# Optimization experiments

Measured on AMD Instinct MI355X. Metric: run time of the kernel, lower is better.

Reference implementation:

```python
import jax, jax.numpy as jnp
import numpy as np

B = 4096       # batch
N_IN = 784     # input neurons
BANKS = 64     # banks per layer
L = 16         # layers of banks (layer 0 = input banks)
FAN = 8        # fan-out per source bank into next layer
D = 10         # n_neurons_per_hidd_bank
N_CONN = (L - 1) * BANKS * FAN  # total bank connections (7680)


def setup_inputs() -> dict:
    key = jax.random.key(0)
    ks = jax.random.split(key, 7)
    x = jax.random.normal(ks[0], (B, N_IN), jnp.float32)
    # input2hidden: Linear(N_IN, D, bias=True) for each input bank -> weight [D, N_IN]
    Wi = jax.random.normal(ks[1], (BANKS, D, N_IN), jnp.float32) / np.sqrt(N_IN).astype(np.float32)
    bi = jax.random.normal(ks[2], (BANKS, D), jnp.float32) * 0.1
    # per-edge gate: Linear(D, 1, bias=True); bias shifted so gates are a mix of open/closed
    Wg = jax.random.normal(ks[3], (L - 1, BANKS, FAN, D), jnp.float32) / np.sqrt(D).astype(np.float32)
    bg = jax.random.normal(ks[4], (L - 1, BANKS, FAN), jnp.float32) * 0.3 + 0.2
    # per-edge data: Linear(D, D, bias=False) -> weight [out=D, in=D]
    Wd = jax.random.normal(ks[5], (L - 1, BANKS, FAN, D, D), jnp.float32) / np.sqrt(D).astype(np.float32)
    # hidden2output: Linear(D, 1, bias=False) per output bank
    Wo = jax.random.normal(ks[6], (BANKS, D), jnp.float32) / np.sqrt(D).astype(np.float32)
    return {"x": x, "Wi": Wi, "bi": bi, "Wg": Wg, "bg": bg, "Wd": Wd, "Wo": Wo}


def reference(x, Wi, bi, Wg, bg, Wd, Wo):
    # forward_softgate with defaults: no batch norm, dropout p=0 (identity),
    # gates enabled (b_no_gates=False), positive gate loss, no gate_status.
    batch = x.shape[0]
    # static scatter targets: source bank s feeds banks (s+k)%BANKS of next layer
    s = np.arange(BANKS)[:, None]
    k = np.arange(FAN)[None, :]
    tgt = jnp.asarray(((s + k) % BANKS).reshape(-1))  # [BANKS*FAN]

    # input banks (layer 0); the target loop applies ReLU to every bank, incl. input banks
    acts = jax.nn.relu(jnp.einsum('bi,koi->bko', x, Wi) + bi)  # [B, BANKS, D]

    def layer(acts, w):
        wg, bgl, wd = w
        # gate: hardtanh(Linear(acts), 0, 1) per edge -> [B, BANKS, FAN]
        gate = jnp.clip(jnp.einsum('bsd,skd->bsk', acts, wg) + bgl, 0.0, 1.0)
        # data: Linear(D, D, bias=False); torch y = x @ W.T with W[out, in]
        data = jnp.einsum('bsd,sked->bske', acts, wd)  # [B, BANKS, FAN, D]
        contrib = (gate[..., None] * data).reshape(batch, BANKS * FAN, D)
        acc = jnp.zeros_like(acts).at[:, tgt].add(contrib)  # scatter-add into target banks
        new_acts = jax.nn.relu(acc)
        gate_sum = gate.sum(axis=(1, 2))                   # per-sample gate activity
        n_open = (gate > 0.0).sum().astype(jnp.float32)    # open-gate count
        return new_acts, (gate_sum, n_open)

    acts, (gate_sums, n_opens) = jax.lax.scan(layer, acts, (Wg, bg, Wd))
    total_gate_act = (gate_sums.sum(axis=0) / N_CONN)[:, None]          # [B, 1]
    prob_open_gate = n_opens.sum() / (N_CONN * batch)                   # scalar
    # output banks = last layer banks, Linear(D,1,bias=False) each, then ReLU
    output = jax.nn.relu(jnp.einsum('bkd,kd->bk', acts, Wo))            # [B, BANKS]
    return output, total_gate_act, prob_open_gate
```

## Files before the change

kernel.cpp:

```cpp
#include <hip/hip_runtime.h>
#include <type_traits>

#define NIN 784
#define BANKS 64
#define NLAYER 15
#define FAN 8
#define DD 10
#define NBF 640
#define NSW 4
#define NSB 8

typedef float f32x2 __attribute__((ext_vector_type(2)));

#define BM 128
#define BN 64
#define BK 16

__global__ __launch_bounds__(256)
void input_gemm(const float* __restrict__ x, const float* __restrict__ Wi,
                const float* __restrict__ bi, float* __restrict__ acts)
{
    __shared__ float As[BK][BM + 4];
    __shared__ float Bs[BK][BN + 4];
    const int tid = threadIdx.x;
    const int tx = tid & 15, ty = tid >> 4;
    const int m0 = blockIdx.x * BM;
    const int n0 = blockIdx.y * BN;

    f32x2 acc2[8][2];
#pragma unroll
    for (int i = 0; i < 8; ++i)
#pragma unroll
        for (int j = 0; j < 2; ++j) acc2[i][j] = f32x2{0.f, 0.f};

    for (int kb = 0; kb < NIN / BK; ++kb) {
#pragma unroll
        for (int i = 0; i < 2; ++i) {
            int flat = tid + 256 * i;
            int m = flat >> 2, kq = flat & 3;
            float4 v = *(const float4*)(x + (m0 + m) * NIN + kb * BK + kq * 4);
            As[kq*4+0][m] = v.x; As[kq*4+1][m] = v.y;
            As[kq*4+2][m] = v.z; As[kq*4+3][m] = v.w;
        }
        {
            int n = tid >> 2, kq = tid & 3;
            float4 v = *(const float4*)(Wi + (n0 + n) * NIN + kb * BK + kq * 4);
            Bs[kq*4+0][n] = v.x; Bs[kq*4+1][n] = v.y;
            Bs[kq*4+2][n] = v.z; Bs[kq*4+3][n] = v.w;
        }
        __syncthreads();
#pragma unroll
        for (int k = 0; k < BK; ++k) {
            float4 a0 = *(const float4*)(&As[k][ty*8]);
            float4 a1 = *(const float4*)(&As[k][ty*8+4]);
            float4 bb = *(const float4*)(&Bs[k][tx*4]);
            float av[8] = {a0.x,a0.y,a0.z,a0.w,a1.x,a1.y,a1.z,a1.w};
            f32x2 bv2[2] = { f32x2{bb.x, bb.y}, f32x2{bb.z, bb.w} };
#pragma unroll
            for (int i = 0; i < 8; ++i) {
                f32x2 ai = f32x2{av[i], av[i]};
#pragma unroll
                for (int j = 0; j < 2; ++j)
                    acc2[i][j] = __builtin_elementwise_fma(ai, bv2[j], acc2[i][j]);
            }
        }
        __syncthreads();
    }
    float4 bv = *(const float4*)(bi + n0 + tx*4);
#pragma unroll
    for (int i = 0; i < 8; ++i) {
        int row = m0 + ty*8 + i;
        float4 o;
        o.x = fmaxf(acc2[i][0][0] + bv.x, 0.f);
        o.y = fmaxf(acc2[i][0][1] + bv.y, 0.f);
        o.z = fmaxf(acc2[i][1][0] + bv.z, 0.f);
        o.w = fmaxf(acc2[i][1][1] + bv.w, 0.f);
        *(float4*)(acts + row * NBF + n0 + tx*4) = o;
    }
}

__device__ __forceinline__ float f4c_rt(const float4& v, int c) {
    return c == 0 ? v.x : (c == 1 ? v.y : (c == 2 ? v.z : v.w));
}

typedef const __attribute__((address_space(1))) void gas_void;
typedef __attribute__((address_space(3))) void las_void;

__device__ __forceinline__ void gll16(const void* g, void* l) {
    __builtin_amdgcn_global_load_lds((gas_void*)g, (las_void*)l, 16, 0, 0);
}

#define NCH (NLAYER*FAN*28*64)
#define NBI (NLAYER*2*64)

__global__ __launch_bounds__(256)
void transpose_weights(const float* __restrict__ Wg, const float* __restrict__ bg,
                       const float* __restrict__ Wd,
                       float4* __restrict__ chunk_t, float4* __restrict__ bias_t)
{
    int tid = blockIdx.x * 256 + threadIdx.x;
    if (tid < NCH) {
        int b = tid & 63;
        int rk = tid >> 6;
        int r = rk % 28;
        int lk = rk / 28;
        int k = lk & 7;
        int l = lk >> 3;
        float4 v;
        if (r < 25) {
            v = ((const float4*)Wd)[(((size_t)(l*64+b)*8 + k)*25) + r];
        } else {
            int q = r - 25;
            size_t base = ((size_t)(l*64+b)*8 + k)*10 + 4*q;
            float t[4];
#pragma unroll
            for (int c = 0; c < 4; ++c)
                t[c] = (4*q + c < 10) ? Wg[base + c] : 0.f;
            v = make_float4(t[0], t[1], t[2], t[3]);
        }
        chunk_t[tid] = v;
    } else if (tid < NCH + NBI) {
        int t2 = tid - NCH;
        int b = t2 & 63;
        int q = (t2 >> 6) & 1;
        int l = t2 >> 7;
        bias_t[t2] = ((const float4*)bg)[(size_t)(l*64+b)*2 + q];
    }
}

__global__ __launch_bounds__(256, 2)
void routenet_v9(const float* __restrict__ acts0,
                 const float4* __restrict__ chunk_t, const float4* __restrict__ bias_t,
                 const float* __restrict__ Wo,
                 float* __restrict__ out, unsigned int* __restrict__ nopen_g)
{
    __shared__ float4 wdstage[2][28][64];
    __shared__ float4 biasbuf[2][2][64];
    __shared__ float  exch[2][NSW][5][64];

    const int tid  = threadIdx.x;
    const int lane = tid & 63;
    const int w    = tid >> 6;
    const int g    = w & 1;
    const int h    = w >> 1;
    const int b0   = blockIdx.x * NSB + g * NSW;

    f32x2 A2[2][DD];
#pragma unroll
    for (int p = 0; p < 2; ++p) {
        const float2* q0 = (const float2*)(acts0 + (size_t)(b0 + 2*p    ) * NBF + lane * DD);
        const float2* q1 = (const float2*)(acts0 + (size_t)(b0 + 2*p + 1) * NBF + lane * DD);
#pragma unroll
        for (int d2 = 0; d2 < 5; ++d2) {
            float2 v0 = q0[d2], v1 = q1[d2];
            A2[p][2*d2  ] = f32x2{v0.x, v1.x};
            A2[p][2*d2+1] = f32x2{v0.y, v1.y};
        }
    }

    f32x2 gs2[2] = { f32x2{0.f,0.f}, f32x2{0.f,0.f} };
    unsigned int nop = 0;

    auto stage_chunk = [&](int l, int k, int pdst) {
        const float4* base = chunk_t + (size_t)(l*8 + k) * 28 * 64;
#pragma unroll
        for (int j = 0; j < 7; ++j) {
            int r = w + 4 * j;
            gll16(base + r*64 + lane, &wdstage[pdst][r][0]);
        }
    };
    auto stage_bias = [&](int l) {
        int q = w & 1;
        gll16(bias_t + (size_t)(l*2 + q)*64 + lane, &biasbuf[l & 1][q][0]);
    };

    stage_chunk(0, 0, 0);
    stage_bias(0);
    asm volatile("s_waitcnt vmcnt(0)" ::: "memory");
    asm volatile("s_barrier" ::: "memory");

    for (int l = 0; l < NLAYER; ++l) {
        const int lp = l & 1;
        f32x2 acc2[2][5];
#pragma unroll
        for (int p = 0; p < 2; ++p)
#pragma unroll
            for (int el = 0; el < 5; ++el) acc2[p][el] = f32x2{0.f, 0.f};

        auto chunk_body = [&](auto Hc, int k, int p) {
            constexpr int H = Hc.value;
            float4 wgq[3];
#pragma unroll
            for (int q = 0; q < 3; ++q) wgq[q] = wdstage[p][25 + q][lane];
            const float bias = f4c_rt(biasbuf[lp][(k >> 2) & 1][lane], k & 3);
            float wgv[DD];
#pragma unroll
            for (int d = 0; d < DD; ++d) wgv[d] = f4c_rt(wgq[d >> 2], d & 3);

            f32x2 gz[2];
#pragma unroll
            for (int pp = 0; pp < 2; ++pp) {
                f32x2 z = f32x2{bias, bias};
#pragma unroll
                for (int d = 0; d < DD; ++d)
                    z = __builtin_elementwise_fma(A2[pp][d], f32x2{wgv[d], wgv[d]}, z);
                f32x2 gate = __builtin_elementwise_min(
                                 __builtin_elementwise_max(z, f32x2{0.f, 0.f}),
                                 f32x2{1.f, 1.f});
                if (H == 0) {
                    gs2[pp] += gate;
                    nop += (z[0] > 0.f) ? 1u : 0u;
                    nop += (z[1] > 0.f) ? 1u : 0u;
                }
                gz[pp] = gate;
            }

            float4 wv[13];
#pragma unroll
            for (int i = 0; i < 13; ++i) wv[i] = wdstage[p][12*H + i][lane];

            const int src = (lane - k) & 63;
#pragma unroll
            for (int el = 0; el < 5; ++el) {
#pragma unroll
                for (int pp = 0; pp < 2; ++pp) {
                    f32x2 dot = f32x2{0.f, 0.f};
#pragma unroll
                    for (int d = 0; d < DD; ++d) {
                        const int idx = (5*H + el) * 10 + d - 48*H;
                        const float wd = f4c_rt(wv[idx >> 2], idx & 3);
                        dot = __builtin_elementwise_fma(A2[pp][d], f32x2{wd, wd}, dot);
                    }
                    f32x2 cc = gz[pp] * dot;
                    f32x2 r;
                    r[0] = __shfl(cc[0], src, 64);
                    r[1] = __shfl(cc[1], src, 64);
                    acc2[pp][el] += r;
                }
            }
        };

#pragma unroll
        for (int c = 0; c < 8; ++c) {
            const int p = c & 1;
            if (c < 7) {
                stage_chunk(l, c + 1, p ^ 1);
                asm volatile("s_waitcnt vmcnt(7)" ::: "memory");
            } else if (l + 1 < NLAYER) {
                stage_chunk(l + 1, 0, p ^ 1);
                stage_bias(l + 1);
                asm volatile("s_waitcnt vmcnt(8)" ::: "memory");
            } else {
                asm volatile("s_waitcnt vmcnt(0)" ::: "memory");
            }
            asm volatile("s_barrier" ::: "memory");

            if (h == 0) chunk_body(std::integral_constant<int,0>{}, c, p);
            else        chunk_body(std::integral_constant<int,1>{}, c, p);

            if (c < 7) {
                asm volatile("s_waitcnt lgkmcnt(0)" ::: "memory");
                asm volatile("s_barrier" ::: "memory");
            }
        }

        if (h == 0) {
#pragma unroll
            for (int s = 0; s < NSW; ++s)
#pragma unroll
                for (int el = 0; el < 5; ++el)
                    A2[s>>1][el][s&1] = fmaxf(acc2[s>>1][el][s&1], 0.f);
        } else {
#pragma unroll
            for (int s = 0; s < NSW; ++s)
#pragma unroll
                for (int el = 0; el < 5; ++el) {
                    float v = fmaxf(acc2[s>>1][el][s&1], 0.f);
                    A2[s>>1][5 + el][s&1] = v;
                    exch[g][s][el][lane] = v;
                }
        }
        asm volatile("s_waitcnt lgkmcnt(0)" ::: "memory");
        asm volatile("s_barrier" ::: "memory");

        if (h == 0) {
#pragma unroll
            for (int s = 0; s < NSW; ++s)
#pragma unroll
                for (int el = 0; el < 5; ++el)
                    A2[s>>1][5 + el][s&1] = exch[g][s][el][lane];
            if (l + 1 < NLAYER) {
#pragma unroll
                for (int s = 0; s < NSW; ++s)
#pragma unroll
                    for (int el = 0; el < 5; ++el)
                        exch[g][s][el][lane] = A2[s>>1][el][s&1];
            }
        }
        if (l + 1 < NLAYER) {
            asm volatile("s_waitcnt lgkmcnt(0)" ::: "memory");
            asm volatile("s_barrier" ::: "memory");
            if (h == 1) {
#pragma unroll
                for (int s = 0; s < NSW; ++s)
#pragma unroll
                    for (int el = 0; el < 5; ++el)
                        A2[s>>1][el][s&1] = exch[g][s][el][lane];
            }
        }
    }

    if (h == 0) {
        float wo[DD];
        const float2* pw = (const float2*)(Wo + lane * DD);
#pragma unroll
        for (int d2 = 0; d2 < 5; ++d2) {
            float2 v = pw[d2];
            wo[2*d2] = v.x; wo[2*d2+1] = v.y;
        }
#pragma unroll
        for (int p = 0; p < 2; ++p) {
            f32x2 o = f32x2{0.f, 0.f};
#pragma unroll
            for (int d = 0; d < DD; ++d)
                o = __builtin_elementwise_fma(A2[p][d], f32x2{wo[d], wo[d]}, o);
            out[(size_t)(b0 + 2*p    ) * BANKS + lane] = fmaxf(o[0], 0.f);
            out[(size_t)(b0 + 2*p + 1) * BANKS + lane] = fmaxf(o[1], 0.f);
        }

#pragma unroll
        for (int s = 0; s < NSW; ++s) {
            float v = gs2[s>>1][s&1];
#pragma unroll
            for (int off = 32; off; off >>= 1) v += __shfl_xor(v, off, 64);
            if (lane == 0)
                out[(size_t)4096 * BANKS + b0 + s] = v * (1.0f / 7680.0f);
        }
        {
            unsigned int v = nop;
#pragma unroll
            for (int off = 32; off; off >>= 1) v += __shfl_xor(v, off, 64);
            if (lane == 0) atomicAdd(nopen_g, v);
        }
    }
}

__global__ __launch_bounds__(256, 2)
void routenet_v5f(const float* __restrict__ acts0,
                  const float* __restrict__ x, const float* __restrict__ Wi,
                  const float* __restrict__ bi,
                  const float* __restrict__ Wg, const float* __restrict__ bg,
                  const float* __restrict__ Wd, const float* __restrict__ Wo,
                  float* __restrict__ out, unsigned int* __restrict__ nopen_g)
{
    __shared__ float4 wdstage[2][28][64];
    __shared__ float4 biasbuf[2][2][64];
    __shared__ float  exch[2][NSW][5][64];

    const int tid  = threadIdx.x;
    const int lane = tid & 63;
    const int w    = tid >> 6;
    const int g    = w & 1;
    const int h    = w >> 1;
    const int b0   = blockIdx.x * NSB + g * NSW;

    float a[NSW][DD];

    if (acts0) {
#pragma unroll
        for (int s = 0; s < NSW; ++s) {
            const float2* p = (const float2*)(acts0 + (size_t)(b0 + s) * NBF + lane * DD);
#pragma unroll
            for (int d2 = 0; d2 < 5; ++d2) {
                float2 v = p[d2];
                a[s][d2*2]   = v.x;
                a[s][d2*2+1] = v.y;
            }
        }
    } else {
        for (int s = 0; s < NSW; ++s) {
            const float* xb2 = x + (size_t)(b0 + s) * NIN;
            for (int d = 0; d < DD; ++d) {
                int n = lane * DD + d;
                const float* wr = Wi + (size_t)n * NIN;
                float z = bi[n];
                for (int i = 0; i < NIN; ++i) z = fmaf(xb2[i], wr[i], z);
                a[s][d] = fmaxf(z, 0.f);
            }
        }
    }

    float gsum[NSW];
#pragma unroll
    for (int s = 0; s < NSW; ++s) gsum[s] = 0.f;
    unsigned int nop = 0;

    auto stage_chunk = [&](int l, int k, int pdst) {
        const float* wd_base = Wd + (size_t)l * (BANKS*FAN*DD*DD)
                                  + (size_t)lane * (FAN*DD*DD) + k * (DD*DD);
        const float* wg_base = Wg + (size_t)l * (BANKS*FAN*DD)
                                  + lane * (FAN*DD) + ((10*k) >> 2) * 4;
#pragma unroll
        for (int j = 0; j < 7; ++j) {
            int r = w + 4 * j;
            if (r < 25) gll16(wd_base + r * 4, &wdstage[pdst][r][0]);
            else        gll16(wg_base + (r - 25) * 4, &wdstage[pdst][r][0]);
        }
    };
    auto stage_bias = [&](int l) {
        int q = w & 1;
        gll16(bg + (size_t)l * (BANKS*FAN) + lane * FAN + q * 4,
              &biasbuf[l & 1][q][0]);
    };

    stage_chunk(0, 0, 0);
    stage_bias(0);
    asm volatile("s_waitcnt vmcnt(0)" ::: "memory");
    asm volatile("s_barrier" ::: "memory");

    for (int l = 0; l < NLAYER; ++l) {
        const int lp = l & 1;
        float acc[NSW][5];
#pragma unroll
        for (int s = 0; s < NSW; ++s)
#pragma unroll
            for (int el = 0; el < 5; ++el) acc[s][el] = 0.f;

        auto chunk_body = [&](auto Hc, int k, int p) {
            constexpr int H = Hc.value;
            float4 wgq[3];
#pragma unroll
            for (int q = 0; q < 3; ++q) wgq[q] = wdstage[p][25 + q][lane];
            const float bias = f4c_rt(biasbuf[lp][(k >> 2) & 1][lane], k & 3);
            float wgv[DD];
            if ((k & 1) == 0) {
#pragma unroll
                for (int d = 0; d < DD; ++d) wgv[d] = f4c_rt(wgq[d >> 2], d & 3);
            } else {
#pragma unroll
                for (int d = 0; d < DD; ++d) wgv[d] = f4c_rt(wgq[(d+2) >> 2], (d+2) & 3);
            }

            float gz[NSW];
#pragma unroll
            for (int s = 0; s < NSW; ++s) {
                float z = bias;
#pragma unroll
                for (int d = 0; d < DD; ++d) z = fmaf(a[s][d], wgv[d], z);
                float gate = fminf(fmaxf(z, 0.f), 1.f);
                if (H == 0) { gsum[s] += gate; nop += (z > 0.f) ? 1u : 0u; }
                gz[s] = gate;
            }

            float4 wv[13];
#pragma unroll
            for (int i = 0; i < 13; ++i) wv[i] = wdstage[p][12*H + i][lane];

            const int src = (lane - k) & 63;
#pragma unroll
            for (int el = 0; el < 5; ++el) {
#pragma unroll
                for (int s = 0; s < NSW; ++s) {
                    float dot = 0.f;
#pragma unroll
                    for (int d = 0; d < DD; ++d) {
                        const int idx = (5*H + el) * 10 + d - 48*H;
                        dot = fmaf(a[s][d], f4c_rt(wv[idx >> 2], idx & 3), dot);
                    }
                    acc[s][el] += __shfl(gz[s] * dot, src, 64);
                }
            }
        };

#pragma unroll
        for (int c = 0; c < 8; ++c) {
            const int p = c & 1;
            if (c < 7) {
                stage_chunk(l, c + 1, p ^ 1);
                asm volatile("s_waitcnt vmcnt(7)" ::: "memory");
            } else if (l + 1 < NLAYER) {
                stage_chunk(l + 1, 0, p ^ 1);
                stage_bias(l + 1);
                asm volatile("s_waitcnt vmcnt(8)" ::: "memory");
            } else {
                asm volatile("s_waitcnt vmcnt(0)" ::: "memory");
            }
            asm volatile("s_barrier" ::: "memory");

            if (h == 0) chunk_body(std::integral_constant<int,0>{}, c, p);
            else        chunk_body(std::integral_constant<int,1>{}, c, p);

            if (c < 7) {
                asm volatile("s_waitcnt lgkmcnt(0)" ::: "memory");
                asm volatile("s_barrier" ::: "memory");
            }
        }

        if (h == 0) {
#pragma unroll
            for (int s = 0; s < NSW; ++s)
#pragma unroll
                for (int el = 0; el < 5; ++el)
                    a[s][el] = fmaxf(acc[s][el], 0.f);
        } else {
#pragma unroll
            for (int s = 0; s < NSW; ++s)
#pragma unroll
                for (int el = 0; el < 5; ++el) {
                    a[s][5 + el] = fmaxf(acc[s][el], 0.f);
                    exch[g][s][el][lane] = a[s][5 + el];
                }
        }
        asm volatile("s_waitcnt lgkmcnt(0)" ::: "memory");
        asm volatile("s_barrier" ::: "memory");

        if (h == 0) {
#pragma unroll
            for (int s = 0; s < NSW; ++s)
#pragma unroll
                for (int el = 0; el < 5; ++el)
                    a[s][5 + el] = exch[g][s][el][lane];
            if (l + 1 < NLAYER) {
#pragma unroll
                for (int s = 0; s < NSW; ++s)
#pragma unroll
                    for (int el = 0; el < 5; ++el)
                        exch[g][s][el][lane] = a[s][el];
            }
        }
        if (l + 1 < NLAYER) {
            asm volatile("s_waitcnt lgkmcnt(0)" ::: "memory");
            asm volatile("s_barrier" ::: "memory");
            if (h == 1) {
#pragma unroll
                for (int s = 0; s < NSW; ++s)
#pragma unroll
                    for (int el = 0; el < 5; ++el)
                        a[s][el] = exch[g][s][el][lane];
            }
        }
    }

    if (h == 0) {
        float wo[DD];
        const float2* p = (const float2*)(Wo + lane * DD);
#pragma unroll
        for (int d2 = 0; d2 < 5; ++d2) {
            float2 v = p[d2];
            wo[d2*2] = v.x; wo[d2*2+1] = v.y;
        }
#pragma unroll
        for (int s = 0; s < NSW; ++s) {
            float v = 0.f;
#pragma unroll
            for (int d = 0; d < DD; ++d) v = fmaf(a[s][d], wo[d], v);
            out[(size_t)(b0 + s) * BANKS + lane] = fmaxf(v, 0.f);
        }

#pragma unroll
        for (int s = 0; s < NSW; ++s) {
            float v = gsum[s];
#pragma unroll
            for (int off = 32; off; off >>= 1) v += __shfl_xor(v, off, 64);
            if (lane == 0)
                out[(size_t)4096 * BANKS + b0 + s] = v * (1.0f / 7680.0f);
        }
        {
            unsigned int v = nop;
#pragma unroll
            for (int off = 32; off; off >>= 1) v += __shfl_xor(v, off, 64);
            if (lane == 0) atomicAdd(nopen_g, v);
        }
    }
}

__global__ void finalize_prob(const unsigned int* __restrict__ nopen,
                              float* __restrict__ out)
{
    out[4096*64 + 4096] = (float)(*nopen) / 31457280.0f;
}

extern "C" void kernel_launch(void* const* d_in, const int* in_sizes, int n_in,
                              void* d_out, int out_size, void* d_ws, size_t ws_size,
                              hipStream_t stream)
{
    const float* x  = (const float*)d_in[0];
    const float* Wi = (const float*)d_in[1];
    const float* bi = (const float*)d_in[2];
    const float* Wg = (const float*)d_in[3];
    const float* bg = (const float*)d_in[4];
    const float* Wd = (const float*)d_in[5];
    const float* Wo = (const float*)d_in[6];
    float* out = (float*)d_out;

    const size_t ACTS_BYTES  = (size_t)4096 * NBF * 4;
    const size_t CHUNK_BYTES = (size_t)NCH * 16;
    const size_t BIAS_BYTES  = (size_t)NBI * 16;
    const size_t FULL_BYTES  = ACTS_BYTES + CHUNK_BYTES + BIAS_BYTES + 64;

    bool full    = ws_size >= FULL_BYTES;
    bool actonly = !full && ws_size >= ACTS_BYTES + 64;

    float* acts0 = (full || actonly) ? (float*)d_ws : nullptr;
    float4* chunk_t = full ? (float4*)((char*)d_ws + ACTS_BYTES) : nullptr;
    float4* bias_t  = full ? (float4*)((char*)d_ws + ACTS_BYTES + CHUNK_BYTES) : nullptr;
    unsigned int* nopen = full
        ? (unsigned int*)((char*)d_ws + ACTS_BYTES + CHUNK_BYTES + BIAS_BYTES)
        : (actonly ? (unsigned int*)((char*)d_ws + ACTS_BYTES)
                   : (unsigned int*)d_ws);

    hipMemsetAsync(nopen, 0, 4, stream);

    if (acts0) {
        dim3 grid(4096 / BM, NBF / BN);
        input_gemm<<<grid, 256, 0, stream>>>(x, Wi, bi, acts0);
    }
    if (full) {
        transpose_weights<<<(NCH + NBI + 255) / 256, 256, 0, stream>>>(
            Wg, bg, Wd, chunk_t, bias_t);
        routenet_v9<<<4096 / NSB, 256, 0, stream>>>(
            acts0, chunk_t, bias_t, Wo, out, nopen);
    } else {
        routenet_v5f<<<4096 / NSB, 256, 0, stream>>>(
            acts0, x, Wi, bi, Wg, bg, Wd, Wo, out, nopen);
    }
    finalize_prob<<<1, 1, 0, stream>>>(nopen, out);
}
```

Baseline: 298.1 us.

## Fuse input GEMM with weight transpose and cut a per-layer barrier

```diff
diff --git a/kernel.cpp b/kernel.cpp
--- a/kernel.cpp
+++ b/kernel.cpp
@@ -12,73 +12,6 @@
 
 typedef float f32x2 __attribute__((ext_vector_type(2)));
 
-#define BM 128
-#define BN 64
-#define BK 16
-
-__global__ __launch_bounds__(256)
-void input_gemm(const float* __restrict__ x, const float* __restrict__ Wi,
-                const float* __restrict__ bi, float* __restrict__ acts)
-{
-    __shared__ float As[BK][BM + 4];
-    __shared__ float Bs[BK][BN + 4];
-    const int tid = threadIdx.x;
-    const int tx = tid & 15, ty = tid >> 4;
-    const int m0 = blockIdx.x * BM;
-    const int n0 = blockIdx.y * BN;
-
-    f32x2 acc2[8][2];
-#pragma unroll
-    for (int i = 0; i < 8; ++i)
-#pragma unroll
-        for (int j = 0; j < 2; ++j) acc2[i][j] = f32x2{0.f, 0.f};
-
-    for (int kb = 0; kb < NIN / BK; ++kb) {
-#pragma unroll
-        for (int i = 0; i < 2; ++i) {
-            int flat = tid + 256 * i;
-            int m = flat >> 2, kq = flat & 3;
-            float4 v = *(const float4*)(x + (m0 + m) * NIN + kb * BK + kq * 4);
-            As[kq*4+0][m] = v.x; As[kq*4+1][m] = v.y;
-            As[kq*4+2][m] = v.z; As[kq*4+3][m] = v.w;
-        }
-        {
-            int n = tid >> 2, kq = tid & 3;
-            float4 v = *(const float4*)(Wi + (n0 + n) * NIN + kb * BK + kq * 4);
-            Bs[kq*4+0][n] = v.x; Bs[kq*4+1][n] = v.y;
-            Bs[kq*4+2][n] = v.z; Bs[kq*4+3][n] = v.w;
-        }
-        __syncthreads();
-#pragma unroll
-        for (int k = 0; k < BK; ++k) {
-            float4 a0 = *(const float4*)(&As[k][ty*8]);
-            float4 a1 = *(const float4*)(&As[k][ty*8+4]);
-            float4 bb = *(const float4*)(&Bs[k][tx*4]);
-            float av[8] = {a0.x,a0.y,a0.z,a0.w,a1.x,a1.y,a1.z,a1.w};
-            f32x2 bv2[2] = { f32x2{bb.x, bb.y}, f32x2{bb.z, bb.w} };
-#pragma unroll
-            for (int i = 0; i < 8; ++i) {
-                f32x2 ai = f32x2{av[i], av[i]};
-#pragma unroll
-                for (int j = 0; j < 2; ++j)
-                    acc2[i][j] = __builtin_elementwise_fma(ai, bv2[j], acc2[i][j]);
-            }
-        }
-        __syncthreads();
-    }
-    float4 bv = *(const float4*)(bi + n0 + tx*4);
-#pragma unroll
-    for (int i = 0; i < 8; ++i) {
-        int row = m0 + ty*8 + i;
-        float4 o;
-        o.x = fmaxf(acc2[i][0][0] + bv.x, 0.f);
-        o.y = fmaxf(acc2[i][0][1] + bv.y, 0.f);
-        o.z = fmaxf(acc2[i][1][0] + bv.z, 0.f);
-        o.w = fmaxf(acc2[i][1][1] + bv.w, 0.f);
-        *(float4*)(acts + row * NBF + n0 + tx*4) = o;
-    }
-}
-
 __device__ __forceinline__ float f4c_rt(const float4& v, int c) {
     return c == 0 ? v.x : (c == 1 ? v.y : (c == 2 ? v.z : v.w));
 }
@@ -92,51 +25,109 @@
 
 #define NCH (NLAYER*FAN*28*64)
 #define NBI (NLAYER*2*64)
+#define GEMM_BLKS 640
+#define TR_BLKS   848
 
 __global__ __launch_bounds__(256)
-void transpose_weights(const float* __restrict__ Wg, const float* __restrict__ bg,
-                       const float* __restrict__ Wd,
-                       float4* __restrict__ chunk_t, float4* __restrict__ bias_t)
+void fused_prologue(const float* __restrict__ x, const float* __restrict__ Wi,
+                    const float* __restrict__ bi,
+                    const float* __restrict__ Wg, const float* __restrict__ bg,
+                    const float* __restrict__ Wd,
+                    float* __restrict__ acts,
+                    float4* __restrict__ chunk_t, float4* __restrict__ bias_t)
 {
-    int tid = blockIdx.x * 256 + threadIdx.x;
-    if (tid < NCH) {
-        int b = tid & 63;
-        int rk = tid >> 6;
-        int r = rk % 28;
-        int lk = rk / 28;
-        int k = lk & 7;
-        int l = lk >> 3;
-        float4 v;
-        if (r < 25) {
-            v = ((const float4*)Wd)[(((size_t)(l*64+b)*8 + k)*25) + r];
-        } else {
-            int q = r - 25;
-            size_t base = ((size_t)(l*64+b)*8 + k)*10 + 4*q;
-            float t[4];
-#pragma unroll
-            for (int c = 0; c < 4; ++c)
-                t[c] = (4*q + c < 10) ? Wg[base + c] : 0.f;
-            v = make_float4(t[0], t[1], t[2], t[3]);
-        }
-        chunk_t[tid] = v;
-    } else if (tid < NCH + NBI) {
-        int t2 = tid - NCH;
-        int b = t2 & 63;
-        int q = (t2 >> 6) & 1;
-        int l = t2 >> 7;
-        bias_t[t2] = ((const float4*)bg)[(size_t)(l*64+b)*2 + q];
+    if (blockIdx.x >= GEMM_BLKS) {
+        int tid = (blockIdx.x - GEMM_BLKS) * 256 + threadIdx.x;
+        if (tid < NCH) {
+            int b = tid & 63;
+            int rk = tid >> 6;
+            int r = rk % 28;
+            int lk = rk / 28;
+            int k = lk & 7;
+            int l = lk >> 3;
+            float4 v;
+            if (r < 25) {
+                v = ((const float4*)Wd)[(((size_t)(l*64+b)*8 + k)*25) + r];
+            } else {
+                int q = r - 25;
+                size_t base = ((size_t)(l*64+b)*8 + k)*10 + 4*q;
+                float t[4];
+#pragma unroll
+                for (int c = 0; c < 4; ++c)
+                    t[c] = (4*q + c < 10) ? Wg[base + c] : 0.f;
+                v = make_float4(t[0], t[1], t[2], t[3]);
+            }
+            chunk_t[tid] = v;
+        } else if (tid < NCH + NBI) {
+            int t2 = tid - NCH;
+            int b = t2 & 63;
+            int q = (t2 >> 6) & 1;
+            int l = t2 >> 7;
+            bias_t[t2] = ((const float4*)bg)[(size_t)(l*64+b)*2 + q];
+        }
+        return;
+    }
+
+    __shared__ float As[16][68];
+    __shared__ float Bs[16][68];
+    const int tid = threadIdx.x;
+    const int tx = tid & 15, ty = tid >> 4;
+    const int m0 = (blockIdx.x & 63) * 64;
+    const int n0 = (blockIdx.x >> 6) * 64;
+
+    float acc[4][4];
+#pragma unroll
+    for (int i = 0; i < 4; ++i)
+#pragma unroll
+        for (int j = 0; j < 4; ++j) acc[i][j] = 0.f;
+
+    for (int kb = 0; kb < NIN / 16; ++kb) {
+        {
+            int m = tid >> 2, kq = tid & 3;
+            float4 v = *(const float4*)(x + (m0 + m) * NIN + kb * 16 + kq * 4);
+            As[kq*4+0][m] = v.x; As[kq*4+1][m] = v.y;
+            As[kq*4+2][m] = v.z; As[kq*4+3][m] = v.w;
+            float4 u = *(const float4*)(Wi + (n0 + m) * NIN + kb * 16 + kq * 4);
+            Bs[kq*4+0][m] = u.x; Bs[kq*4+1][m] = u.y;
+            Bs[kq*4+2][m] = u.z; Bs[kq*4+3][m] = u.w;
+        }
+        __syncthreads();
+#pragma unroll
+        for (int k = 0; k < 16; ++k) {
+            float4 a4 = *(const float4*)(&As[k][ty*4]);
+            float4 b4 = *(const float4*)(&Bs[k][tx*4]);
+            float av[4] = {a4.x, a4.y, a4.z, a4.w};
+            float bv[4] = {b4.x, b4.y, b4.z, b4.w};
+#pragma unroll
+            for (int i = 0; i < 4; ++i)
+#pragma unroll
+                for (int j = 0; j < 4; ++j)
+                    acc[i][j] = fmaf(av[i], bv[j], acc[i][j]);
+        }
+        __syncthreads();
+    }
+    float4 bv = *(const float4*)(bi + n0 + tx*4);
+#pragma unroll
+    for (int i = 0; i < 4; ++i) {
+        int row = m0 + ty*4 + i;
+        float4 o;
+        o.x = fmaxf(acc[i][0] + bv.x, 0.f);
+        o.y = fmaxf(acc[i][1] + bv.y, 0.f);
+        o.z = fmaxf(acc[i][2] + bv.z, 0.f);
+        o.w = fmaxf(acc[i][3] + bv.w, 0.f);
+        *(float4*)(acts + row * NBF + n0 + tx*4) = o;
     }
 }
 
 __global__ __launch_bounds__(256, 2)
-void routenet_v9(const float* __restrict__ acts0,
-                 const float4* __restrict__ chunk_t, const float4* __restrict__ bias_t,
-                 const float* __restrict__ Wo,
-                 float* __restrict__ out, unsigned int* __restrict__ nopen_g)
+void routenet_v10(const float* __restrict__ acts0,
+                  const float4* __restrict__ chunk_t, const float4* __restrict__ bias_t,
+                  const float* __restrict__ Wo,
+                  float* __restrict__ out, unsigned int* __restrict__ nopen_g)
 {
     __shared__ float4 wdstage[2][28][64];
-    __shared__ float4 biasbuf[2][2][64];
-    __shared__ float  exch[2][NSW][5][64];
+    __shared__ float  exH1[2][NSW][5][64];
+    __shared__ float  exH0[2][NSW][5][64];
 
     const int tid  = threadIdx.x;
     const int lane = tid & 63;
@@ -169,18 +160,20 @@
             gll16(base + r*64 + lane, &wdstage[pdst][r][0]);
         }
     };
-    auto stage_bias = [&](int l) {
-        int q = w & 1;
-        gll16(bias_t + (size_t)(l*2 + q)*64 + lane, &biasbuf[l & 1][q][0]);
-    };
 
     stage_chunk(0, 0, 0);
-    stage_bias(0);
+    float4 bq0 = bias_t[lane];
+    float4 bq1 = bias_t[64 + lane];
     asm volatile("s_waitcnt vmcnt(0)" ::: "memory");
     asm volatile("s_barrier" ::: "memory");
 
     for (int l = 0; l < NLAYER; ++l) {
-        const int lp = l & 1;
+        float4 bn0 = bq0, bn1 = bq1;
+        if (l + 1 < NLAYER) {
+            bn0 = bias_t[(size_t)((l+1)*2    ) * 64 + lane];
+            bn1 = bias_t[(size_t)((l+1)*2 + 1) * 64 + lane];
+        }
+
         f32x2 acc2[2][5];
 #pragma unroll
         for (int p = 0; p < 2; ++p)
@@ -192,7 +185,7 @@
             float4 wgq[3];
 #pragma unroll
             for (int q = 0; q < 3; ++q) wgq[q] = wdstage[p][25 + q][lane];
-            const float bias = f4c_rt(biasbuf[lp][(k >> 2) & 1][lane], k & 3);
+            const float bias = f4c_rt((k & 4) ? bq1 : bq0, k & 3);
             float wgv[DD];
 #pragma unroll
             for (int d = 0; d < DD; ++d) wgv[d] = f4c_rt(wgq[d >> 2], d & 3);
@@ -248,15 +241,26 @@
                 asm volatile("s_waitcnt vmcnt(7)" ::: "memory");
             } else if (l + 1 < NLAYER) {
                 stage_chunk(l + 1, 0, p ^ 1);
-                stage_bias(l + 1);
-                asm volatile("s_waitcnt vmcnt(8)" ::: "memory");
+                asm volatile("s_waitcnt vmcnt(7)" ::: "memory");
             } else {
                 asm volatile("s_waitcnt vmcnt(0)" ::: "memory");
             }
+            if (c == 0) {
+                asm volatile("s_waitcnt lgkmcnt(0)" ::: "memory");
+            }
             asm volatile("s_barrier" ::: "memory");
 
+            __builtin_amdgcn_s_setprio(1);
+            if (c == 0 && l > 0 && h == 1) {
+#pragma unroll
+                for (int s = 0; s < NSW; ++s)
+#pragma unroll
+                    for (int el = 0; el < 5; ++el)
+                        A2[s>>1][el][s&1] = exH0[g][s][el][lane];
+            }
             if (h == 0) chunk_body(std::integral_constant<int,0>{}, c, p);
             else        chunk_body(std::integral_constant<int,1>{}, c, p);
+            __builtin_amdgcn_s_setprio(0);
 
             if (c < 7) {
                 asm volatile("s_waitcnt lgkmcnt(0)" ::: "memory");
@@ -277,7 +281,7 @@
                 for (int el = 0; el < 5; ++el) {
                     float v = fmaxf(acc2[s>>1][el][s&1], 0.f);
                     A2[s>>1][5 + el][s&1] = v;
-                    exch[g][s][el][lane] = v;
+                    exH1[g][s][el][lane] = v;
                 }
         }
         asm volatile("s_waitcnt lgkmcnt(0)" ::: "memory");
@@ -288,26 +292,16 @@
             for (int s = 0; s < NSW; ++s)
 #pragma unroll
                 for (int el = 0; el < 5; ++el)
-                    A2[s>>1][5 + el][s&1] = exch[g][s][el][lane];
+                    A2[s>>1][5 + el][s&1] = exH1[g][s][el][lane];
             if (l + 1 < NLAYER) {
 #pragma unroll
                 for (int s = 0; s < NSW; ++s)
 #pragma unroll
                     for (int el = 0; el < 5; ++el)
-                        exch[g][s][el][lane] = A2[s>>1][el][s&1];
-            }
-        }
-        if (l + 1 < NLAYER) {
-            asm volatile("s_waitcnt lgkmcnt(0)" ::: "memory");
-            asm volatile("s_barrier" ::: "memory");
-            if (h == 1) {
-#pragma unroll
-                for (int s = 0; s < NSW; ++s)
-#pragma unroll
-                    for (int el = 0; el < 5; ++el)
-                        A2[s>>1][el][s&1] = exch[g][s][el][lane];
-            }
-        }
+                        exH0[g][s][el][lane] = A2[s>>1][el][s&1];
+            }
+        }
+        bq0 = bn0; bq1 = bn1;
     }
 
     if (h == 0) {
@@ -611,16 +605,16 @@
 
     hipMemsetAsync(nopen, 0, 4, stream);
 
-    if (acts0) {
-        dim3 grid(4096 / BM, NBF / BN);
-        input_gemm<<<grid, 256, 0, stream>>>(x, Wi, bi, acts0);
-    }
     if (full) {
-        transpose_weights<<<(NCH + NBI + 255) / 256, 256, 0, stream>>>(
-            Wg, bg, Wd, chunk_t, bias_t);
-        routenet_v9<<<4096 / NSB, 256, 0, stream>>>(
+        fused_prologue<<<GEMM_BLKS + TR_BLKS, 256, 0, stream>>>(
+            x, Wi, bi, Wg, bg, Wd, acts0, chunk_t, bias_t);
+        routenet_v10<<<4096 / NSB, 256, 0, stream>>>(
             acts0, chunk_t, bias_t, Wo, out, nopen);
     } else {
+        if (acts0) {
+            fused_prologue<<<GEMM_BLKS, 256, 0, stream>>>(
+                x, Wi, bi, Wg, bg, Wd, acts0, nullptr, nullptr);
+        }
         routenet_v5f<<<4096 / NSB, 256, 0, stream>>>(
             acts0, x, Wi, bi, Wg, bg, Wd, Wo, out, nopen);
     }
```

New measurement: 281.2 us. 5.7% less time.
